# Kernel optimization log

Measured on AMD Instinct MI355X. Metric: run time of the kernel, lower is better.

Reference implementation:

```python
import jax, jax.numpy as jnp
import numpy as np

IN_SIZE = 1024   # reconstruction / detector size (circle=True -> grid_size == in_size == it_size)
N_THETA = 180    # default theta = arange(180) degrees


def _ramp_fourier_filter(size):
    # torch-skimage style spatial-domain ramp filter, then rfft (RampFilter._get_fourier_filter)
    n = jnp.concatenate([jnp.arange(1, size // 2 + 1, 2),
                         jnp.arange(size // 2 - 1, 0, -2)]).astype(jnp.float32)
    f = jnp.zeros((size,), jnp.float32)
    f = f.at[0].set(0.25)
    f = f.at[1::2].set(-1.0 / (jnp.pi * n) ** 2)
    return 2.0 * jnp.fft.rfft(f)  # complex (size//2+1,)


def _filter_sinogram(x):
    # filter along detector axis (dim=-2). x: (B,C,H,A)
    H = x.shape[2]
    padded = max(64, int(2 ** np.ceil(np.log2(2 * H))))  # 2048 for H=1024
    xp = jnp.pad(x, ((0, 0), (0, 0), (0, padded - H), (0, 0)))
    filt = _ramp_fourier_filter(padded)[None, None, :, None]  # unsqueeze(-1) in torch
    proj = jnp.fft.rfft(xp, axis=2) * filt
    return jnp.fft.irfft(proj, n=padded, axis=2)[:, :, :H, :]


def _backproject(xf):
    # grid_sample (bilinear, zeros padding, align_corners=False) + sum over angles,
    # done separably: (1) interp along angle axis (X grid coord is constant per angle),
    # (2) per-angle gather along detector axis via lax.scan accumulation (avoids the
    # huge (B,C,S,A,S) intermediate the torch code materializes).
    B, C, H, A = xf.shape
    S = H  # grid_size == it_size for circle=True

    # --- angle-axis bilinear weights: X_a = a*2/(A-1)-1 -> ix = a*A/(A-1) - 0.5 ---
    a = jnp.arange(A, dtype=jnp.float32)
    ix = a * (A / (A - 1)) - 0.5
    i0 = jnp.floor(ix).astype(jnp.int32)
    fx = ix - i0
    i1 = i0 + 1
    w0 = jnp.where((i0 >= 0) & (i0 < A), 1.0 - fx, 0.0)
    w1 = jnp.where((i1 >= 0) & (i1 < A), fx, 0.0)
    xa = (xf[:, :, :, jnp.clip(i0, 0, A - 1)] * w0
          + xf[:, :, :, jnp.clip(i1, 0, A - 1)] * w1)  # (B,C,H,A)

    unit = jnp.linspace(-1.0, 1.0, S)
    xg = unit[None, :]   # xgrid varies along width (meshgrid 'ij' second output)
    yg = unit[:, None]   # ygrid varies along height
    theta_rad = jnp.arange(A, dtype=jnp.float32) * (jnp.pi / 180.0)

    def step(acc, inp):
        v, t = inp                                  # v: (B,C,H), t: scalar rad
        T = xg * jnp.cos(t) - yg * jnp.sin(t)       # (S,S) normalized detector coord
        iy = ((T + 1.0) * H - 1.0) * 0.5            # align_corners=False unnormalize
        j0 = jnp.floor(iy).astype(jnp.int32)
        fy = iy - j0
        j1 = j0 + 1
        u0 = jnp.where((j0 >= 0) & (j0 < H), 1.0 - fy, 0.0)
        u1 = jnp.where((j1 >= 0) & (j1 < H), fy, 0.0)
        s = (v[:, :, jnp.clip(j0, 0, H - 1)] * u0
             + v[:, :, jnp.clip(j1, 0, H - 1)] * u1)  # (B,C,S,S)
        return acc + s, None

    acc0 = jnp.zeros((B, C, S, S), xf.dtype)
    reco, _ = jax.lax.scan(step, acc0, (jnp.moveaxis(xa, 3, 0), theta_rad))

    circ = (xg ** 2 + yg ** 2) <= 1.0               # reconstruction circle mask
    return jnp.where(circ, reco, 0.0) * (jnp.pi / (2 * A))


def reference(x):
    xf = _filter_sinogram(x)
    return _backproject(xf)


def setup_inputs() -> dict:
    key = jax.random.key(0)
    x = jax.random.normal(key, (16, 1, IN_SIZE, N_THETA), dtype=jnp.float32)
    return {"x": x}
```

## Files before the change

### kernel.cpp

```cpp
#include <hip/hip_runtime.h>
#include <math.h>

#define HH 1024
#define AA 180
#define BB 16
#define NCOL (BB*AA)
#define RSP 1028
#define GUARD 48
#define RS 1120
#define PI_D 3.14159265358979323846

#define GANG 45
#define WIN 48

#define OFF_CG   0
#define OFF_CST  512
#define OFF_CST2 1232
#define OFF_DATA 1600

__device__ __forceinline__ float fractf_(float x) {
#if __has_builtin(__builtin_amdgcn_fractf)
    return __builtin_amdgcn_fractf(x);
#else
    return x - floorf(x);
#endif
}

__global__ __launch_bounds__(512) void k_tables(float* __restrict__ ws) {
    int t = threadIdx.x;
    if (t < 512) {
        double d = 2.0 * t + 1.0;
        ws[OFF_CG + t] = (float)(-2.0 / (PI_D * PI_D * d * d));
    }
    if (t < AA) {
        float thf = (float)t * 0.017453292519943295f;
        double th = (double)thf;
        double c = cos(th), s = sin(th);
        float4* cst4 = (float4*)(ws + OFF_CST);
        cst4[t] = make_float4((float)(512.0 * c), (float)(512.0 * s),
                              (float)(-(8192.0 / 1023.0) * s), 0.f);
        float2* cst2 = (float2*)(ws + OFF_CST2);
        cst2[t] = make_float2((float)(512.0 * c), (float)(512.0 * s));
    }
}

__device__ __forceinline__ void filter_core(const float* __restrict__ x,
                                            const float* __restrict__ cg,
                                            float* xsp, int t, int col,
                                            float acc[16]) {
    int b = col / AA, a = col - b * AA;

    float4* z4 = (float4*)xsp;
    #pragma unroll
    for (int i = t; i < 816; i += 64) z4[i] = make_float4(0.f, 0.f, 0.f, 0.f);
    __syncthreads();

    float ixf = (float)a * (float)(180.0/179.0) - 0.5f;
    float fl = floorf(ixf);
    int i0 = (int)fl;
    float fx = ixf - fl;
    float w0 = (i0 >= 0)      ? (1.0f - fx) : 0.0f;
    float w1 = (i0 + 1 < AA)  ? fx          : 0.0f;
    int c0 = max(i0, 0);
    int c1 = min(i0 + 1, AA - 1);
    const float* xb = x + (size_t)b * HH * AA;
    for (int i = t; i < HH; i += 64) {
        float v = w0 * xb[i * AA + c0] + w1 * xb[i * AA + c1];
        int q = 1024 + i;
        xsp[q + (q >> 4)] = v;
    }
    __syncthreads();

    int pp = 17 * t;
    float Lw[16], Rw[16];
    #pragma unroll
    for (int m = 0; m < 16; ++m) {
        int f = 1024 + m;
        acc[m] = 0.5f * xsp[pp + f + (f >> 4)];
    }
    #pragma unroll
    for (int m = 0; m < 16; ++m) {
        int f = 1 + m;
        Lw[(m + 1) & 15] = xsp[pp + f + (f >> 4)];
        int g = 2047 + m;
        Rw[(m - 1) & 15] = xsp[pp + g + (g >> 4)];
    }

    for (int it0 = 0; it0 < 512; it0 += 8) {
        #pragma unroll
        for (int u = 0; u < 8; ++u) {
            int it = it0 + u;
            float cv = cg[511 - it];
            #pragma unroll
            for (int m = 0; m < 16; ++m) {
                acc[m] = fmaf(cv, Lw[(m + 2*u + 1) & 15] + Rw[(m - 2*u - 1) & 15], acc[m]);
            }
            int fL  = 2*it + 17;
            Lw[(2*u + 1) & 15] = xsp[pp + fL  + (fL  >> 4)];
            int fL2 = 2*it + 18;
            Lw[(2*u + 2) & 15] = xsp[pp + fL2 + (fL2 >> 4)];
            int fR  = 2045 - 2*it;
            Rw[(13 - 2*u) & 15] = xsp[pp + fR  + (fR  >> 4)];
            int fR2 = 2046 - 2*it;
            Rw[(14 - 2*u) & 15] = xsp[pp + fR2 + (fR2 >> 4)];
        }
    }
}

__global__ __launch_bounds__(64) void k_filter_pair(const float* __restrict__ x,
                                                    const float* __restrict__ cg,
                                                    float2* __restrict__ pair) {
    __shared__ float xsp[3264];
    int t = threadIdx.x;
    int col = blockIdx.x;
    float acc[16];
    filter_core(x, cg, xsp, t, col, acc);

    const float SC = (float)(PI_D / 360.0);
    float yv[16];
    #pragma unroll
    for (int m = 0; m < 16; ++m) yv[m] = acc[m] * SC;
    float ynext = __shfl_down(yv[0], 1);
    if (t == 63) ynext = 0.f;

    float2* rowp = pair + (size_t)col * RSP;
    int s0 = 16 * t + 2;
    #pragma unroll
    for (int m = 0; m < 15; ++m) rowp[s0 + m] = make_float2(yv[m], yv[m + 1]);
    rowp[s0 + 15] = make_float2(yv[15], ynext);
    if (t == 0) {
        rowp[0] = make_float2(0.f, 0.f);
        rowp[1] = make_float2(0.f, yv[0]);
    }
    if (t == 63) rowp[1026] = make_float2(0.f, 0.f);
}

__global__ __launch_bounds__(256, 4) void k_bproj_lds(const float* __restrict__ ws,
                                                      const float2* __restrict__ pair,
                                                      float* __restrict__ out) {
    __shared__ float2 win[GANG * WIN];
    __shared__ int   baseL[GANG];
    __shared__ float bfL[GANG];

    const float4* cst = (const float4*)(ws + OFF_CST);
    int t = threadIdx.x;
    int n = blockIdx.x;
    int b    = (n & 7) + 8 * ((n >> 3) & 1);
    int tile = n >> 4;
    int bx = tile & 31;
    int by = tile >> 5;
    int tx = t & 31;
    int ty = t >> 5;
    int xg = bx * 32 + tx;
    int y0 = by * 32;
    int yg = y0 + ty;

    const float DEL = (float)(2.0 / 1023.0);
    float ux  = __fadd_rn(__fmul_rn((float)xg, DEL), -1.0f);
    float uy  = __fadd_rn(__fmul_rn((float)yg, DEL), -1.0f);
    float nuy = -uy;

    float cxl = __fadd_rn(__fmul_rn((float)(bx*32),      DEL), -1.0f);
    float cxh = __fadd_rn(__fmul_rn((float)(bx*32 + 31), DEL), -1.0f);
    float cyl = __fadd_rn(__fmul_rn((float)(y0),         DEL), -1.0f);
    float cyh = __fadd_rn(__fmul_rn((float)(y0 + 31),    DEL), -1.0f);

    float minax = (cxl <= 0.f && cxh >= 0.f) ? 0.f : fminf(fabsf(cxl), fabsf(cxh));
    float minay = (cyl <= 0.f && cyh >= 0.f) ? 0.f : fminf(fabsf(cyl), fabsf(cyh));
    float rmin2 = minax * minax + minay * minay;
    float maxax = fmaxf(fabsf(cxl), fabsf(cxh));
    float maxay = fmaxf(fabsf(cyl), fabsf(cyh));
    float rmax2 = maxax * maxax + maxay * maxay;

    size_t o0 = ((size_t)b << 20) + ((size_t)yg << 10) + (size_t)xg;
    float* p0 = out + o0;

    if (rmin2 > 1.000001f) {
        p0[0] = 0.f; p0[8 << 10] = 0.f; p0[16 << 10] = 0.f; p0[24 << 10] = 0.f;
        return;
    }

    bool interior = (rmax2 <= 0.9999f);
    const float2* slab = pair + (size_t)b * (AA * RSP);
    float a0 = 0.f, a1 = 0.f, a2 = 0.f, a3 = 0.f;
    float nyl = -cyl, nyh = -cyh;

    for (int g0 = 0; g0 < AA; g0 += GANG) {
        if (t < GANG) {
            float4 cs = cst[g0 + t];
            float mpx = fminf(cxl * cs.x, cxh * cs.x);
            float mpy = fminf(nyl * cs.y, nyh * cs.y);
            float minP = mpx + mpy + 513.5f;
            int base = (int)floorf(minP) - 1;
            base = min(max(base, 0), 1027 - WIN);
            baseL[t] = base;
            bfL[t] = 513.5f - (float)base;
        }
        __syncthreads();

        for (int idx = t; idx < GANG * WIN; idx += 256) {
            int al = idx / WIN;
            int w  = idx - WIN * al;
            const float2* rp = slab + (size_t)(g0 + al) * RSP;
            win[idx] = rp[baseL[al] + w];
        }
        __syncthreads();

        if (interior) {
            #pragma unroll 3
            for (int g = 0; g < GANG; ++g) {
                float4 cs = cst[g0 + g];
                float bf = bfL[g];
                float P0 = fmaf(ux, cs.x, fmaf(nuy, cs.y, bf));
                float P1 = P0 + cs.z;
                float P2 = fmaf(2.0f, cs.z, P0);
                float P3 = P2 + cs.z;
                int j0 = (int)P0, j1 = (int)P1, j2 = (int)P2, j3 = (int)P3;
                const float2* wg = win + g * WIN;
                float2 d0 = wg[j0];
                float2 d1 = wg[j1];
                float2 d2 = wg[j2];
                float2 d3 = wg[j3];
                float f0 = fractf_(P0), f1 = fractf_(P1), f2v = fractf_(P2), f3 = fractf_(P3);
                a0 = fmaf(f0, d0.y - d0.x, a0 + d0.x);
                a1 = fmaf(f1, d1.y - d1.x, a1 + d1.x);
                a2 = fmaf(f2v, d2.y - d2.x, a2 + d2.x);
                a3 = fmaf(f3, d3.y - d3.x, a3 + d3.x);
            }
        } else {
            #pragma unroll 3
            for (int g = 0; g < GANG; ++g) {
                float4 cs = cst[g0 + g];
                float bf = bfL[g];
                float P0 = fmaf(ux, cs.x, fmaf(nuy, cs.y, bf));
                float P1 = P0 + cs.z;
                float P2 = fmaf(2.0f, cs.z, P0);
                float P3 = P2 + cs.z;
                int j0 = (int)P0, j1 = (int)P1, j2 = (int)P2, j3 = (int)P3;
                j0 = min(max(j0, 0), WIN - 1); j1 = min(max(j1, 0), WIN - 1);
                j2 = min(max(j2, 0), WIN - 1); j3 = min(max(j3, 0), WIN - 1);
                const float2* wg = win + g * WIN;
                float2 d0 = wg[j0];
                float2 d1 = wg[j1];
                float2 d2 = wg[j2];
                float2 d3 = wg[j3];
                float f0 = fractf_(P0), f1 = fractf_(P1), f2v = fractf_(P2), f3 = fractf_(P3);
                a0 = fmaf(f0, d0.y - d0.x, a0 + d0.x);
                a1 = fmaf(f1, d1.y - d1.x, a1 + d1.x);
                a2 = fmaf(f2v, d2.y - d2.x, a2 + d2.x);
                a3 = fmaf(f3, d3.y - d3.x, a3 + d3.x);
            }
        }
        __syncthreads();
    }

    if (interior) {
        p0[0] = a0; p0[8 << 10] = a1; p0[16 << 10] = a2; p0[24 << 10] = a3;
    } else {
        float uy1 = __fadd_rn(__fmul_rn((float)(yg + 8),  DEL), -1.0f);
        float uy2 = __fadd_rn(__fmul_rn((float)(yg + 16), DEL), -1.0f);
        float uy3 = __fadd_rn(__fmul_rn((float)(yg + 24), DEL), -1.0f);
        float xx = __fmul_rn(ux, ux);
        float r20 = __fadd_rn(xx, __fmul_rn(uy,  uy));
        float r21 = __fadd_rn(xx, __fmul_rn(uy1, uy1));
        float r22 = __fadd_rn(xx, __fmul_rn(uy2, uy2));
        float r23 = __fadd_rn(xx, __fmul_rn(uy3, uy3));
        p0[0]        = (r20 <= 1.0f) ? a0 : 0.f;
        p0[8 << 10]  = (r21 <= 1.0f) ? a1 : 0.f;
        p0[16 << 10] = (r22 <= 1.0f) ? a2 : 0.f;
        p0[24 << 10] = (r23 <= 1.0f) ? a3 : 0.f;
    }
}

__global__ __launch_bounds__(64) void k_filter_sc(const float* __restrict__ x,
                                                  const float* __restrict__ cg,
                                                  float* __restrict__ xaf) {
    __shared__ float xsp[3264];
    int t = threadIdx.x;
    int col = blockIdx.x;
    float acc[16];
    filter_core(x, cg, xsp, t, col, acc);

    const float SC = (float)(PI_D / 360.0);
    float* rb = xaf + (size_t)col * RS;
    if (t < 12)            ((float4*)rb)[t]              = make_float4(0.f,0.f,0.f,0.f);
    else if (t < 24)       ((float4*)rb)[268 + (t - 12)] = make_float4(0.f,0.f,0.f,0.f);
    float4* o4 = (float4*)(rb + GUARD + 16 * t);
    #pragma unroll
    for (int m4 = 0; m4 < 4; ++m4)
        o4[m4] = make_float4(acc[4*m4]*SC, acc[4*m4+1]*SC, acc[4*m4+2]*SC, acc[4*m4+3]*SC);
}

__global__ __launch_bounds__(256, 4) void k_bproj_sc(const float* __restrict__ ws,
                                                     const float* __restrict__ xaf,
                                                     float* __restrict__ out) {
    const float2* cst2 = (const float2*)(ws + OFF_CST2);
    int t = threadIdx.x;
    int tx = t & 15, ty = t >> 4;
    int bx = blockIdx.x, by = blockIdx.y, b = blockIdx.z;
    int xg = bx * 16 + tx, yg = by * 16 + ty;
    const float DEL = (float)(2.0 / 1023.0);
    float ux = __fadd_rn(__fmul_rn((float)xg, DEL), -1.0f);
    float uy = __fadd_rn(__fmul_rn((float)yg, DEL), -1.0f);

    float cx0 = __fadd_rn(__fmul_rn((float)(bx*16),      DEL), -1.0f);
    float cx1 = __fadd_rn(__fmul_rn((float)(bx*16 + 15), DEL), -1.0f);
    float cy0 = __fadd_rn(__fmul_rn((float)(by*16),      DEL), -1.0f);
    float cy1 = __fadd_rn(__fmul_rn((float)(by*16 + 15), DEL), -1.0f);
    float minax = (cx0 <= 0.f && cx1 >= 0.f) ? 0.f : fminf(fabsf(cx0), fabsf(cx1));
    float minay = (cy0 <= 0.f && cy1 >= 0.f) ? 0.f : fminf(fabsf(cy0), fabsf(cy1));
    float rmin2 = minax * minax + minay * minay;

    size_t oidx = ((size_t)b << 20) + ((size_t)yg << 10) + (size_t)xg;
    if (rmin2 > 1.000001f) { out[oidx] = 0.f; return; }

    const float* row = xaf + (size_t)b * (AA * RS);
    const float BIAS = 511.5f + (float)GUARD;
    float nuy = -uy;
    float acc = 0.f;

    #pragma unroll 4
    for (int a = 0; a < AA; ++a) {
        float2 cs = cst2[a];
        float iy = fmaf(ux, cs.x, fmaf(nuy, cs.y, BIAS));
        int j = (int)iy;
        float fy = fractf_(iy);
        float v0 = row[j];
        float v1 = row[j + 1];
        acc = fmaf(fy, v1 - v0, acc + v0);
        row += RS;
    }

    float r2 = __fadd_rn(__fmul_rn(ux, ux), __fmul_rn(uy, uy));
    out[oidx] = (r2 <= 1.0f) ? acc : 0.f;
}

extern "C" void kernel_launch(void* const* d_in, const int* in_sizes, int n_in,
                              void* d_out, int out_size, void* d_ws, size_t ws_size,
                              hipStream_t stream) {
    const float* x = (const float*)d_in[0];
    float* out = (float*)d_out;
    float* ws = (float*)d_ws;
    float* cg  = ws + OFF_CG;

    hipLaunchKernelGGL(k_tables, dim3(1), dim3(512), 0, stream, ws);

    size_t need_pair = (size_t)OFF_DATA * 4 + (size_t)NCOL * RSP * sizeof(float2);
    if (ws_size >= need_pair) {
        float2* pair = (float2*)(ws + OFF_DATA);
        hipLaunchKernelGGL(k_filter_pair, dim3(NCOL), dim3(64), 0, stream, x, cg, pair);
        hipLaunchKernelGGL(k_bproj_lds, dim3(16384), dim3(256), 0, stream, ws, pair, out);
    } else {
        float* xaf = ws + OFF_DATA;
        hipLaunchKernelGGL(k_filter_sc, dim3(NCOL), dim3(64), 0, stream, x, cg, xaf);
        hipLaunchKernelGGL(k_bproj_sc, dim3(64, 64, BB), dim3(256), 0, stream, ws, xaf, out);
    }
}
```

Before: 651.2 us.

## Store value/delta pairs, stage windows with float4 loads, cache angle constants in LDS

The filter kernel now writes each detector pair as (value, next − value) instead of (value, next). That removes one subtraction per bilinear sample in the backprojection inner loop. The backprojection window base is rounded to an even index so each window can be staged into LDS with 16-byte float4 loads. Per-angle cos/sin/step and the base offset are packed into one LDS float4, which replaces a global constant load plus a separate LDS load. The unroll factor goes from 3 to 5; aligning the base down may reduce how much of the 48-entry window margin covers the tile.

```diff
diff --git a/kernel.cpp b/kernel.cpp
--- a/kernel.cpp
+++ b/kernel.cpp
@@ -126,8 +126,8 @@
     float2* rowp = pair + (size_t)col * RSP;
     int s0 = 16 * t + 2;
     #pragma unroll
-    for (int m = 0; m < 15; ++m) rowp[s0 + m] = make_float2(yv[m], yv[m + 1]);
-    rowp[s0 + 15] = make_float2(yv[15], ynext);
+    for (int m = 0; m < 15; ++m) rowp[s0 + m] = make_float2(yv[m], yv[m + 1] - yv[m]);
+    rowp[s0 + 15] = make_float2(yv[15], ynext - yv[15]);
     if (t == 0) {
         rowp[0] = make_float2(0.f, 0.f);
         rowp[1] = make_float2(0.f, yv[0]);
@@ -138,9 +138,9 @@
 __global__ __launch_bounds__(256, 4) void k_bproj_lds(const float* __restrict__ ws,
                                                       const float2* __restrict__ pair,
                                                       float* __restrict__ out) {
-    __shared__ float2 win[GANG * WIN];
-    __shared__ int   baseL[GANG];
-    __shared__ float bfL[GANG];
+    __shared__ float4 winbuf[GANG * (WIN/2)];
+    __shared__ float4 angf4[GANG];
+    __shared__ int    baseL[GANG];
 
     const float4* cst = (const float4*)(ws + OFF_CST);
     int t = threadIdx.x;
@@ -182,6 +182,7 @@
 
     bool interior = (rmax2 <= 0.9999f);
     const float2* slab = pair + (size_t)b * (AA * RSP);
+    const float2* win = (const float2*)winbuf;
     float a0 = 0.f, a1 = 0.f, a2 = 0.f, a3 = 0.f;
     float nyl = -cyl, nyh = -cyh;
 
@@ -193,28 +194,28 @@
             float minP = mpx + mpy + 513.5f;
             int base = (int)floorf(minP) - 1;
             base = min(max(base, 0), 1027 - WIN);
+            base &= ~1;
             baseL[t] = base;
-            bfL[t] = 513.5f - (float)base;
+            angf4[t] = make_float4(cs.x, cs.y, cs.z, 513.5f - (float)base);
         }
         __syncthreads();
 
-        for (int idx = t; idx < GANG * WIN; idx += 256) {
-            int al = idx / WIN;
-            int w  = idx - WIN * al;
-            const float2* rp = slab + (size_t)(g0 + al) * RSP;
-            win[idx] = rp[baseL[al] + w];
+        for (int idx = t; idx < GANG * (WIN/2); idx += 256) {
+            int al = idx / (WIN/2);
+            int w  = idx - (WIN/2) * al;
+            const float4* rp4 = (const float4*)(slab + (size_t)(g0 + al) * RSP + baseL[al]);
+            winbuf[idx] = rp4[w];
         }
         __syncthreads();
 
         if (interior) {
-            #pragma unroll 3
+            #pragma unroll 5
             for (int g = 0; g < GANG; ++g) {
-                float4 cs = cst[g0 + g];
-                float bf = bfL[g];
-                float P0 = fmaf(ux, cs.x, fmaf(nuy, cs.y, bf));
-                float P1 = P0 + cs.z;
-                float P2 = fmaf(2.0f, cs.z, P0);
-                float P3 = P2 + cs.z;
+                float4 cb = angf4[g];
+                float P0 = fmaf(ux, cb.x, fmaf(nuy, cb.y, cb.w));
+                float P1 = P0 + cb.z;
+                float P2 = fmaf(2.0f, cb.z, P0);
+                float P3 = P2 + cb.z;
                 int j0 = (int)P0, j1 = (int)P1, j2 = (int)P2, j3 = (int)P3;
                 const float2* wg = win + g * WIN;
                 float2 d0 = wg[j0];
@@ -222,20 +223,19 @@
                 float2 d2 = wg[j2];
                 float2 d3 = wg[j3];
                 float f0 = fractf_(P0), f1 = fractf_(P1), f2v = fractf_(P2), f3 = fractf_(P3);
-                a0 = fmaf(f0, d0.y - d0.x, a0 + d0.x);
-                a1 = fmaf(f1, d1.y - d1.x, a1 + d1.x);
-                a2 = fmaf(f2v, d2.y - d2.x, a2 + d2.x);
-                a3 = fmaf(f3, d3.y - d3.x, a3 + d3.x);
+                a0 = fmaf(f0, d0.y, a0 + d0.x);
+                a1 = fmaf(f1, d1.y, a1 + d1.x);
+                a2 = fmaf(f2v, d2.y, a2 + d2.x);
+                a3 = fmaf(f3, d3.y, a3 + d3.x);
             }
         } else {
-            #pragma unroll 3
+            #pragma unroll 5
             for (int g = 0; g < GANG; ++g) {
-                float4 cs = cst[g0 + g];
-                float bf = bfL[g];
-                float P0 = fmaf(ux, cs.x, fmaf(nuy, cs.y, bf));
-                float P1 = P0 + cs.z;
-                float P2 = fmaf(2.0f, cs.z, P0);
-                float P3 = P2 + cs.z;
+                float4 cb = angf4[g];
+                float P0 = fmaf(ux, cb.x, fmaf(nuy, cb.y, cb.w));
+                float P1 = P0 + cb.z;
+                float P2 = fmaf(2.0f, cb.z, P0);
+                float P3 = P2 + cb.z;
                 int j0 = (int)P0, j1 = (int)P1, j2 = (int)P2, j3 = (int)P3;
                 j0 = min(max(j0, 0), WIN - 1); j1 = min(max(j1, 0), WIN - 1);
                 j2 = min(max(j2, 0), WIN - 1); j3 = min(max(j3, 0), WIN - 1);
@@ -245,10 +245,10 @@
                 float2 d2 = wg[j2];
                 float2 d3 = wg[j3];
                 float f0 = fractf_(P0), f1 = fractf_(P1), f2v = fractf_(P2), f3 = fractf_(P3);
-                a0 = fmaf(f0, d0.y - d0.x, a0 + d0.x);
-                a1 = fmaf(f1, d1.y - d1.x, a1 + d1.x);
-                a2 = fmaf(f2v, d2.y - d2.x, a2 + d2.x);
-                a3 = fmaf(f3, d3.y - d3.x, a3 + d3.x);
+                a0 = fmaf(f0, d0.y, a0 + d0.x);
+                a1 = fmaf(f1, d1.y, a1 + d1.x);
+                a2 = fmaf(f2v, d2.y, a2 + d2.x);
+                a3 = fmaf(f3, d3.y, a3 + d3.x);
             }
         }
         __syncthreads();
```

New measurement: 586.4 us. 1.11x faster.
